# Optimization experiments

Hardware: AMD Instinct MI355X
Metric: run time of the kernel (lower is better)

## Reference

```python
import jax, jax.numpy as jnp
import numpy as np

LEVEL = 20            # module default -> 21 max-pool passes, kernels 1x1 .. 41x41 (H,W only)
K_SIG = 10.0          # init arg k: sigmoid weight sharpness
N_POOL = LEVEL + 1    # len(max_pool)
DENOM = N_POOL + 1    # torch: level = len(max_pool) + 1 = 22


def _edge3d(mask):
    # Equivalent to F.conv3d(mask, filt, padding=1) > 0 where filt is the
    # in-plane Laplacian: center 1, 4 H/W-neighbors -0.25, zeros elsewhere.
    p = jnp.pad(mask, ((0, 0), (0, 0), (0, 0), (1, 1), (1, 1)))
    lap = mask - 0.25 * (p[..., :-2, 1:-1] + p[..., 2:, 1:-1]
                         + p[..., 1:-1, :-2] + p[..., 1:-1, 2:])
    return (lap > 0).astype(jnp.float32)


def _mp3(x):
    # stride-1 3x3 max pool over H,W with same padding (pads with -inf like torch MaxPool)
    return jax.lax.reduce_window(x, -jnp.inf, jax.lax.max,
                                 (1, 1, 1, 3, 3), (1, 1, 1, 1, 1),
                                 ((0, 0), (0, 0), (0, 0), (1, 1), (1, 1)))


def _cal_dist(mask):
    edge = _edge3d(mask)  # [B,1,D,H,W] binary
    # maxpool with window (2k+1)x(2k+1) on a binary map == k cascaded 3x3 dilations,
    # so sum_{k=0}^{LEVEL} maxpool_{2k+1}(edge) is computed incrementally.
    def body(i, carry):
        e, acc = carry
        return (_mp3(e), acc + e)
    _, acc = jax.lax.fori_loop(0, N_POOL, body, (edge, jnp.zeros_like(edge)))
    return (DENOM - acc) / DENOM


def setup_inputs() -> dict:
    key = jax.random.key(0)
    k1, k2 = jax.random.split(key)
    outputs = jax.random.uniform(k1, (2, 1, 64, 256, 256), dtype=jnp.float32)
    masks = jax.random.randint(k2, (2, 1, 64, 256, 256), 0, 2, dtype=jnp.int32)
    return {"outputs": outputs, "masks": masks}


def reference(outputs, masks):
    eps = 1e-6
    m = masks.astype(jnp.float32)
    dist = _cal_dist(m)
    weight = jax.lax.stop_gradient(2.0 / (1.0 + jnp.exp(K_SIG * dist)))
    b = outputs.shape[0]
    ow = (outputs.astype(jnp.float32) * weight).reshape(b, -1)
    mw = (m * weight).reshape(b, -1)
    intersect = jnp.sum(ow * m.reshape(b, -1), axis=1)
    input_area = jnp.sum(ow, axis=1)
    target_area = jnp.sum(mw, axis=1)
    batch_loss = 1.0 - 2.0 * intersect / (input_area + target_area + 2.0 * eps)
    batch_loss = jnp.where(target_area == 0, 0.0, batch_loss)
    return batch_loss.mean()
```

## Files before the change

### kernel.cpp

```cpp
#include <hip/hip_runtime.h>
#include <stdint.h>

typedef unsigned long long u64;

#define SLICES 128
#define WPS 1024
#define TOTAL_WORDS (SLICES * WPS)
#define NBLK3 512


__global__ __launch_bounds__(256) void k_pack(const int* __restrict__ masks,
                                              u64* __restrict__ mbits) {
    const int lane = threadIdx.x & 63;
    const int wave = (blockIdx.x * 256 + threadIdx.x) >> 6;
    const int nwaves = (gridDim.x * 256) >> 6;
    #pragma unroll 4
    for (int w = wave; w < TOTAL_WORDS; w += nwaves) {
        int v = masks[(size_t)w * 64 + lane];
        u64 bal = __ballot(v != 0);
        if (lane == 0) mbits[w] = bal;
    }
}

__global__ __launch_bounds__(256) void k_dilate(const u64* __restrict__ mbits,
                                                u64* __restrict__ planes) {
    __shared__ u64 rows[256][5];
    __shared__ u64 tmp[256][5];

    const int t = threadIdx.x;
    const int slice = blockIdx.x;
    const u64* mb = mbits + (size_t)slice * WPS;

    u64 m[4];
    #pragma unroll
    for (int j = 0; j < 4; ++j) { m[j] = mb[t * 4 + j]; rows[t][j] = m[j]; }
    __syncthreads();

    u64 c[4];
    {
        u64 up[4], dn[4];
        #pragma unroll
        for (int j = 0; j < 4; ++j) {
            up[j] = (t > 0)   ? rows[t - 1][j] : 0ull;
            dn[j] = (t < 255) ? rows[t + 1][j] : 0ull;
        }
        #pragma unroll
        for (int j = 0; j < 4; ++j) {
            u64 lf = (m[j] << 1) | (j > 0 ? (m[j - 1] >> 63) : 0ull);
            u64 rt = (m[j] >> 1) | (j < 3 ? (m[j + 1] << 63) : 0ull);
            c[j] = m[j] & ~(up[j] & dn[j] & lf & rt);
        }
    }

    u64 p[5][4];
    #pragma unroll
    for (int pl = 0; pl < 5; ++pl)
        #pragma unroll
        for (int j = 0; j < 4; ++j) p[pl][j] = 0ull;

    __syncthreads();

    for (int k = 1; k <= 20; ++k) {
        u64 h[4];
        #pragma unroll
        for (int j = 0; j < 4; ++j) {
            u64 lf = (c[j] << 1) | (j > 0 ? (c[j - 1] >> 63) : 0ull);
            u64 rt = (c[j] >> 1) | (j < 3 ? (c[j + 1] << 63) : 0ull);
            h[j] = c[j] | lf | rt;
            tmp[t][j] = h[j];
        }
        __syncthreads();
        #pragma unroll
        for (int j = 0; j < 4; ++j) {
            u64 u_ = (t > 0)   ? tmp[t - 1][j] : 0ull;
            u64 d_ = (t < 255) ? tmp[t + 1][j] : 0ull;
            u64 n = h[j] | u_ | d_;
            u64 nw = n & ~c[j];
            c[j] = n;
            #pragma unroll
            for (int pl = 0; pl < 5; ++pl)
                if ((k >> pl) & 1) p[pl][j] |= nw;
        }
        int done = ((c[0] & c[1] & c[2] & c[3]) == 0xFFFFFFFFFFFFFFFFull) ? 1 : 0;
        if (__syncthreads_and(done)) break;
    }

    #pragma unroll
    for (int j = 0; j < 4; ++j) {
        u64 u_ = ~c[j];
        p[0][j] |= u_; p[2][j] |= u_; p[4][j] |= u_;
    }

    #pragma unroll
    for (int pl = 0; pl < 5; ++pl)
        #pragma unroll
        for (int j = 0; j < 4; ++j)
            planes[(size_t)pl * TOTAL_WORDS + (size_t)slice * WPS + t * 4 + j] = p[pl][j];
}

__global__ __launch_bounds__(256) void k_reduce(const float* __restrict__ outputs,
                                               const u64* __restrict__ mbits,
                                               const u64* __restrict__ planes,
                                               float* __restrict__ partials) {
    __shared__ float wtab[22];
    __shared__ float red[4][6];
    const int t = threadIdx.x;
    if (t < 22) wtab[t] = 2.0f / (1.0f + __expf(10.0f * (float)(t + 1) * (1.0f / 22.0f)));
    __syncthreads();

    const int tid = blockIdx.x * 256 + t;
    float s[2][3];
    #pragma unroll
    for (int b = 0; b < 2; ++b) { s[b][0] = s[b][1] = s[b][2] = 0.0f; }

    #pragma unroll
    for (int b = 0; b < 2; ++b) {
        for (int i = 0; i < 8; ++i) {
            int pix4 = b * 1048576 + i * 131072 + tid;
            int pix = pix4 * 4;
            float4 o4 = ((const float4*)outputs)[pix4];
            float ov[4] = {o4.x, o4.y, o4.z, o4.w};
            int widx = pix >> 6;
            int sh = pix & 63;
            u64 mw = mbits[widx];
            u64 p0 = planes[widx];
            u64 p1 = planes[TOTAL_WORDS + widx];
            u64 p2 = planes[2 * TOTAL_WORDS + widx];
            u64 p3 = planes[3 * TOTAL_WORDS + widx];
            u64 p4 = planes[4 * TOTAL_WORDS + widx];
            #pragma unroll
            for (int q = 0; q < 4; ++q) {
                int s2 = sh + q;
                int d0 = (int)((p0 >> s2) & 1ull)
                       | ((int)((p1 >> s2) & 1ull) << 1)
                       | ((int)((p2 >> s2) & 1ull) << 2)
                       | ((int)((p3 >> s2) & 1ull) << 3)
                       | ((int)((p4 >> s2) & 1ull) << 4);
                float w = wtab[d0];
                float ow = ov[q] * w;
                s[b][0] += ow;
                if ((mw >> s2) & 1ull) { s[b][1] += w; s[b][2] += ow; }
            }
        }
    }

    #pragma unroll
    for (int b = 0; b < 2; ++b)
        #pragma unroll
        for (int k = 0; k < 3; ++k) {
            float v = s[b][k];
            #pragma unroll
            for (int off = 32; off > 0; off >>= 1) v += __shfl_down(v, off);
            s[b][k] = v;
        }
    const int lane = t & 63, wv = t >> 6;
    if (lane == 0) {
        #pragma unroll
        for (int b = 0; b < 2; ++b)
            #pragma unroll
            for (int k = 0; k < 3; ++k) red[wv][b * 3 + k] = s[b][k];
    }
    __syncthreads();
    if (t < 6) {
        float v = red[0][t] + red[1][t] + red[2][t] + red[3][t];
        partials[blockIdx.x * 6 + t] = v;
    }
}

__global__ __launch_bounds__(64) void k_fin(const float* __restrict__ partials,
                                            float* __restrict__ out) {
    const int lane = threadIdx.x;
    float s[6] = {0, 0, 0, 0, 0, 0};
    for (int i = lane; i < NBLK3; i += 64)
        #pragma unroll
        for (int k = 0; k < 6; ++k) s[k] += partials[i * 6 + k];
    #pragma unroll
    for (int k = 0; k < 6; ++k) {
        float v = s[k];
        #pragma unroll
        for (int off = 32; off > 0; off >>= 1) v += __shfl_down(v, off);
        s[k] = v;
    }
    if (lane == 0) {
        float loss = 0.0f;
        #pragma unroll
        for (int b = 0; b < 2; ++b) {
            float A = s[b * 3 + 0];
            float T = s[b * 3 + 1];
            float I = s[b * 3 + 2];
            float l = (T == 0.0f) ? 0.0f : (1.0f - 2.0f * I / (A + T + 2e-6f));
            loss += l;
        }
        out[0] = 0.5f * loss;
    }
}

extern "C" void kernel_launch(void* const* d_in, const int* in_sizes, int n_in,
                              void* d_out, int out_size, void* d_ws, size_t ws_size,
                              hipStream_t stream) {
    const float* outputs = (const float*)d_in[0];
    const int* masks = (const int*)d_in[1];
    float* out = (float*)d_out;

    u64* mbits = (u64*)d_ws;
    u64* planes = mbits + TOTAL_WORDS;
    float* partials = (float*)((char*)d_ws + (size_t)6 * TOTAL_WORDS * 8);

    k_pack<<<1024, 256, 0, stream>>>(masks, mbits);
    k_dilate<<<SLICES, 256, 0, stream>>>(mbits, planes);
    k_reduce<<<NBLK3, 256, 0, stream>>>(outputs, mbits, planes, partials);
    k_fin<<<1, 64, 0, stream>>>(partials, out);
}
```

Measured before the change: 115.0 us.

## Fuse pack, dilate, reduce and finalize into one cooperative kernel

Result: slower. 334.8 us (+191.2%).

```diff
diff --git a/kernel.cpp b/kernel.cpp
--- a/kernel.cpp
+++ b/kernel.cpp
@@ -1,197 +1,191 @@
 #include <hip/hip_runtime.h>
+#include <hip/hip_cooperative_groups.h>
 #include <stdint.h>
 
+namespace cg = cooperative_groups;
 typedef unsigned long long u64;
 
 #define SLICES 128
 #define WPS 1024
 #define TOTAL_WORDS (SLICES * WPS)
-#define NBLK3 512
-
-
-__global__ __launch_bounds__(256) void k_pack(const int* __restrict__ masks,
-                                              u64* __restrict__ mbits) {
-    const int lane = threadIdx.x & 63;
-    const int wave = (blockIdx.x * 256 + threadIdx.x) >> 6;
-    const int nwaves = (gridDim.x * 256) >> 6;
-    #pragma unroll 4
-    for (int w = wave; w < TOTAL_WORDS; w += nwaves) {
-        int v = masks[(size_t)w * 64 + lane];
-        u64 bal = __ballot(v != 0);
-        if (lane == 0) mbits[w] = bal;
-    }
-}
-
-__global__ __launch_bounds__(256) void k_dilate(const u64* __restrict__ mbits,
-                                                u64* __restrict__ planes) {
+#define NBLK 512
+
+__global__ __launch_bounds__(256) void bbsd_all(const float* __restrict__ outputs,
+                                                const int* __restrict__ masks,
+                                                u64* __restrict__ mbits,
+                                                u64* __restrict__ planes,
+                                                float* __restrict__ partials,
+                                                float* __restrict__ out) {
     __shared__ u64 rows[256][5];
     __shared__ u64 tmp[256][5];
-
+    __shared__ float wtab[22];
+    __shared__ float red[4][8];
+
+    cg::grid_group grid = cg::this_grid();
     const int t = threadIdx.x;
-    const int slice = blockIdx.x;
-    const u64* mb = mbits + (size_t)slice * WPS;
-
-    u64 m[4];
-    #pragma unroll
-    for (int j = 0; j < 4; ++j) { m[j] = mb[t * 4 + j]; rows[t][j] = m[j]; }
-    __syncthreads();
-
-    u64 c[4];
+    const int lane = t & 63, wv = t >> 6;
+    const int tid = blockIdx.x * 256 + t;
+
+    u64 mword = 0;
     {
-        u64 up[4], dn[4];
+        const int4* mp = (const int4*)masks + (size_t)tid * 16;
+        #pragma unroll
+        for (int j = 0; j < 16; ++j) {
+            int4 v = mp[j];
+            u64 b = (u64)(v.x != 0) | ((u64)(v.y != 0) << 1)
+                  | ((u64)(v.z != 0) << 2) | ((u64)(v.w != 0) << 3);
+            mword |= b << (j * 4);
+        }
+        mbits[tid] = mword;
+    }
+    grid.sync();
+
+    if (blockIdx.x < SLICES) {
+        const u64* mb = mbits + (size_t)blockIdx.x * WPS;
+        u64 m[4];
+        #pragma unroll
+        for (int j = 0; j < 4; ++j) { m[j] = mb[t * 4 + j]; rows[t][j] = m[j]; }
+        __syncthreads();
+
+        u64 c[4];
+        {
+            u64 up[4], dn[4];
+            #pragma unroll
+            for (int j = 0; j < 4; ++j) {
+                up[j] = (t > 0)   ? rows[t - 1][j] : 0ull;
+                dn[j] = (t < 255) ? rows[t + 1][j] : 0ull;
+            }
+            #pragma unroll
+            for (int j = 0; j < 4; ++j) {
+                u64 lf = (m[j] << 1) | (j > 0 ? (m[j - 1] >> 63) : 0ull);
+                u64 rt = (m[j] >> 1) | (j < 3 ? (m[j + 1] << 63) : 0ull);
+                c[j] = m[j] & ~(up[j] & dn[j] & lf & rt);
+            }
+        }
+
+        u64 p[5][4];
+        #pragma unroll
+        for (int pl = 0; pl < 5; ++pl)
+            #pragma unroll
+            for (int j = 0; j < 4; ++j) p[pl][j] = 0ull;
+
+        __syncthreads();
+        for (int k = 1; k <= 20; ++k) {
+            u64 h[4];
+            #pragma unroll
+            for (int j = 0; j < 4; ++j) {
+                u64 lf = (c[j] << 1) | (j > 0 ? (c[j - 1] >> 63) : 0ull);
+                u64 rt = (c[j] >> 1) | (j < 3 ? (c[j + 1] << 63) : 0ull);
+                h[j] = c[j] | lf | rt;
+                tmp[t][j] = h[j];
+            }
+            __syncthreads();
+            #pragma unroll
+            for (int j = 0; j < 4; ++j) {
+                u64 u_ = (t > 0)   ? tmp[t - 1][j] : 0ull;
+                u64 d_ = (t < 255) ? tmp[t + 1][j] : 0ull;
+                u64 n = h[j] | u_ | d_;
+                u64 nw = n & ~c[j];
+                c[j] = n;
+                #pragma unroll
+                for (int pl = 0; pl < 5; ++pl)
+                    if ((k >> pl) & 1) p[pl][j] |= nw;
+            }
+            int done = ((c[0] & c[1] & c[2] & c[3]) == 0xFFFFFFFFFFFFFFFFull) ? 1 : 0;
+            if (__syncthreads_and(done)) break;
+        }
+
         #pragma unroll
         for (int j = 0; j < 4; ++j) {
-            up[j] = (t > 0)   ? rows[t - 1][j] : 0ull;
-            dn[j] = (t < 255) ? rows[t + 1][j] : 0ull;
-        }
-        #pragma unroll
-        for (int j = 0; j < 4; ++j) {
-            u64 lf = (m[j] << 1) | (j > 0 ? (m[j - 1] >> 63) : 0ull);
-            u64 rt = (m[j] >> 1) | (j < 3 ? (m[j + 1] << 63) : 0ull);
-            c[j] = m[j] & ~(up[j] & dn[j] & lf & rt);
-        }
-    }
-
-    u64 p[5][4];
-    #pragma unroll
-    for (int pl = 0; pl < 5; ++pl)
-        #pragma unroll
-        for (int j = 0; j < 4; ++j) p[pl][j] = 0ull;
-
-    __syncthreads();
-
-    for (int k = 1; k <= 20; ++k) {
-        u64 h[4];
-        #pragma unroll
-        for (int j = 0; j < 4; ++j) {
-            u64 lf = (c[j] << 1) | (j > 0 ? (c[j - 1] >> 63) : 0ull);
-            u64 rt = (c[j] >> 1) | (j < 3 ? (c[j + 1] << 63) : 0ull);
-            h[j] = c[j] | lf | rt;
-            tmp[t][j] = h[j];
-        }
-        __syncthreads();
-        #pragma unroll
-        for (int j = 0; j < 4; ++j) {
-            u64 u_ = (t > 0)   ? tmp[t - 1][j] : 0ull;
-            u64 d_ = (t < 255) ? tmp[t + 1][j] : 0ull;
-            u64 n = h[j] | u_ | d_;
-            u64 nw = n & ~c[j];
-            c[j] = n;
-            #pragma unroll
-            for (int pl = 0; pl < 5; ++pl)
-                if ((k >> pl) & 1) p[pl][j] |= nw;
-        }
-        int done = ((c[0] & c[1] & c[2] & c[3]) == 0xFFFFFFFFFFFFFFFFull) ? 1 : 0;
-        if (__syncthreads_and(done)) break;
-    }
-
-    #pragma unroll
-    for (int j = 0; j < 4; ++j) {
-        u64 u_ = ~c[j];
-        p[0][j] |= u_; p[2][j] |= u_; p[4][j] |= u_;
-    }
-
-    #pragma unroll
-    for (int pl = 0; pl < 5; ++pl)
-        #pragma unroll
-        for (int j = 0; j < 4; ++j)
-            planes[(size_t)pl * TOTAL_WORDS + (size_t)slice * WPS + t * 4 + j] = p[pl][j];
-}
-
-__global__ __launch_bounds__(256) void k_reduce(const float* __restrict__ outputs,
-                                               const u64* __restrict__ mbits,
-                                               const u64* __restrict__ planes,
-                                               float* __restrict__ partials) {
-    __shared__ float wtab[22];
-    __shared__ float red[4][6];
-    const int t = threadIdx.x;
+            u64 u_ = ~c[j];
+            p[0][j] |= u_; p[2][j] |= u_; p[4][j] |= u_;
+        }
+        #pragma unroll
+        for (int pl = 0; pl < 5; ++pl)
+            #pragma unroll
+            for (int j = 0; j < 4; ++j)
+                planes[(size_t)pl * TOTAL_WORDS + (size_t)blockIdx.x * WPS + t * 4 + j] = p[pl][j];
+        __threadfence();
+    }
+    grid.sync();
+
     if (t < 22) wtab[t] = 2.0f / (1.0f + __expf(10.0f * (float)(t + 1) * (1.0f / 22.0f)));
     __syncthreads();
-
-    const int tid = blockIdx.x * 256 + t;
-    float s[2][3];
-    #pragma unroll
-    for (int b = 0; b < 2; ++b) { s[b][0] = s[b][1] = s[b][2] = 0.0f; }
-
-    #pragma unroll
-    for (int b = 0; b < 2; ++b) {
-        for (int i = 0; i < 8; ++i) {
-            int pix4 = b * 1048576 + i * 131072 + tid;
-            int pix = pix4 * 4;
-            float4 o4 = ((const float4*)outputs)[pix4];
+    {
+        u64 p0 = planes[tid];
+        u64 p1 = planes[TOTAL_WORDS + tid];
+        u64 p2 = planes[2 * TOTAL_WORDS + tid];
+        u64 p3 = planes[3 * TOTAL_WORDS + tid];
+        u64 p4 = planes[4 * TOTAL_WORDS + tid];
+        const float4* op = (const float4*)outputs + (size_t)tid * 16;
+
+        float s0 = 0.0f, s1 = 0.0f, s2 = 0.0f;
+        #pragma unroll
+        for (int j = 0; j < 16; ++j) {
+            float4 o4 = op[j];
             float ov[4] = {o4.x, o4.y, o4.z, o4.w};
-            int widx = pix >> 6;
-            int sh = pix & 63;
-            u64 mw = mbits[widx];
-            u64 p0 = planes[widx];
-            u64 p1 = planes[TOTAL_WORDS + widx];
-            u64 p2 = planes[2 * TOTAL_WORDS + widx];
-            u64 p3 = planes[3 * TOTAL_WORDS + widx];
-            u64 p4 = planes[4 * TOTAL_WORDS + widx];
             #pragma unroll
             for (int q = 0; q < 4; ++q) {
-                int s2 = sh + q;
-                int d0 = (int)((p0 >> s2) & 1ull)
-                       | ((int)((p1 >> s2) & 1ull) << 1)
-                       | ((int)((p2 >> s2) & 1ull) << 2)
-                       | ((int)((p3 >> s2) & 1ull) << 3)
-                       | ((int)((p4 >> s2) & 1ull) << 4);
+                int sh = j * 4 + q;
+                int d0 = (int)((p0 >> sh) & 1ull)
+                       | ((int)((p1 >> sh) & 1ull) << 1)
+                       | ((int)((p2 >> sh) & 1ull) << 2)
+                       | ((int)((p3 >> sh) & 1ull) << 3)
+                       | ((int)((p4 >> sh) & 1ull) << 4);
                 float w = wtab[d0];
                 float ow = ov[q] * w;
-                s[b][0] += ow;
-                if ((mw >> s2) & 1ull) { s[b][1] += w; s[b][2] += ow; }
-            }
-        }
-    }
-
-    #pragma unroll
-    for (int b = 0; b < 2; ++b)
+                float mb = (float)((mword >> sh) & 1ull);
+                s0 += ow;
+                s1 += mb * w;
+                s2 += mb * ow;
+            }
+        }
+        float sv[3] = {s0, s1, s2};
         #pragma unroll
         for (int k = 0; k < 3; ++k) {
-            float v = s[b][k];
+            float v = sv[k];
             #pragma unroll
             for (int off = 32; off > 0; off >>= 1) v += __shfl_down(v, off);
-            s[b][k] = v;
-        }
-    const int lane = t & 63, wv = t >> 6;
-    if (lane == 0) {
-        #pragma unroll
-        for (int b = 0; b < 2; ++b)
-            #pragma unroll
-            for (int k = 0; k < 3; ++k) red[wv][b * 3 + k] = s[b][k];
-    }
-    __syncthreads();
-    if (t < 6) {
-        float v = red[0][t] + red[1][t] + red[2][t] + red[3][t];
-        partials[blockIdx.x * 6 + t] = v;
-    }
-}
-
-__global__ __launch_bounds__(64) void k_fin(const float* __restrict__ partials,
-                                            float* __restrict__ out) {
-    const int lane = threadIdx.x;
-    float s[6] = {0, 0, 0, 0, 0, 0};
-    for (int i = lane; i < NBLK3; i += 64)
-        #pragma unroll
-        for (int k = 0; k < 6; ++k) s[k] += partials[i * 6 + k];
-    #pragma unroll
-    for (int k = 0; k < 6; ++k) {
-        float v = s[k];
-        #pragma unroll
-        for (int off = 32; off > 0; off >>= 1) v += __shfl_down(v, off);
-        s[k] = v;
-    }
-    if (lane == 0) {
-        float loss = 0.0f;
-        #pragma unroll
-        for (int b = 0; b < 2; ++b) {
-            float A = s[b * 3 + 0];
-            float T = s[b * 3 + 1];
-            float I = s[b * 3 + 2];
-            float l = (T == 0.0f) ? 0.0f : (1.0f - 2.0f * I / (A + T + 2e-6f));
-            loss += l;
-        }
-        out[0] = 0.5f * loss;
+            sv[k] = v;
+        }
+        if (lane == 0) { red[wv][0] = sv[0]; red[wv][1] = sv[1]; red[wv][2] = sv[2]; }
+        __syncthreads();
+        if (t < 3) partials[blockIdx.x * 3 + t] =
+            red[0][t] + red[1][t] + red[2][t] + red[3][t];
+        __threadfence();
+    }
+    grid.sync();
+
+    if (blockIdx.x == 0) {
+        float s[6];
+        #pragma unroll
+        for (int k = 0; k < 3; ++k) {
+            s[k]     = partials[t * 3 + k];
+            s[3 + k] = partials[(t + 256) * 3 + k];
+        }
+        #pragma unroll
+        for (int k = 0; k < 6; ++k) {
+            float v = s[k];
+            #pragma unroll
+            for (int off = 32; off > 0; off >>= 1) v += __shfl_down(v, off);
+            s[k] = v;
+        }
+        if (lane == 0) {
+            #pragma unroll
+            for (int k = 0; k < 6; ++k) red[wv][k] = s[k];
+        }
+        __syncthreads();
+        if (t == 0) {
+            float loss = 0.0f;
+            #pragma unroll
+            for (int b = 0; b < 2; ++b) {
+                float A = red[0][b*3+0] + red[1][b*3+0] + red[2][b*3+0] + red[3][b*3+0];
+                float T = red[0][b*3+1] + red[1][b*3+1] + red[2][b*3+1] + red[3][b*3+1];
+                float I = red[0][b*3+2] + red[1][b*3+2] + red[2][b*3+2] + red[3][b*3+2];
+                loss += (T == 0.0f) ? 0.0f : (1.0f - 2.0f * I / (A + T + 2e-6f));
+            }
+            out[0] = 0.5f * loss;
+        }
     }
 }
 
@@ -204,10 +198,10 @@
 
     u64* mbits = (u64*)d_ws;
     u64* planes = mbits + TOTAL_WORDS;
-    float* partials = (float*)((char*)d_ws + (size_t)6 * TOTAL_WORDS * 8);
-
-    k_pack<<<1024, 256, 0, stream>>>(masks, mbits);
-    k_dilate<<<SLICES, 256, 0, stream>>>(mbits, planes);
-    k_reduce<<<NBLK3, 256, 0, stream>>>(outputs, mbits, planes, partials);
-    k_fin<<<1, 64, 0, stream>>>(partials, out);
+    float* partials = (float*)(planes + 5 * TOTAL_WORDS);
+
+    void* args[] = {(void*)&outputs, (void*)&masks, (void*)&mbits,
+                    (void*)&planes, (void*)&partials, (void*)&out};
+    hipLaunchCooperativeKernel((const void*)bbsd_all, dim3(NBLK), dim3(256),
+                               args, 0, stream);
 }
```
